# Kernel optimization log

Measured on AMD Instinct MI355X. Metric: run time of the kernel, lower is better.

## Reference

```python
import jax, jax.numpy as jnp
import numpy as np
import math

N_STFT = 1025
N_MELS = 128
SAMPLE_RATE = 16000
F_MIN = 0.0
F_MAX = 8000.0
MAX_ITER = 20
LR = 0.3
MOMENTUM = 0.9
BATCH = 4
TIME = 1024


def _create_fb_matrix(n_freqs, f_min, f_max, n_mels, sample_rate):
    # Triangular mel filterbank, (n_freqs, n_mels), matching torchaudio's create_fb_matrix.
    all_freqs = np.linspace(0.0, sample_rate // 2, n_freqs)
    m_min = 2595.0 * math.log10(1.0 + f_min / 700.0)
    m_max = 2595.0 * math.log10(1.0 + f_max / 700.0)
    m_pts = np.linspace(m_min, m_max, n_mels + 2)
    f_pts = 700.0 * (10.0 ** (m_pts / 2595.0) - 1.0)
    f_diff = f_pts[1:] - f_pts[:-1]
    slopes = f_pts[None, :] - all_freqs[:, None]  # (n_freqs, n_mels+2)
    down_slopes = -slopes[:, :-2] / f_diff[:-1]
    up_slopes = slopes[:, 2:] / f_diff[1:]
    fb = np.maximum(0.0, np.minimum(down_slopes, up_slopes))
    return jnp.asarray(fb, dtype=jnp.float32)


def setup_inputs() -> dict:
    key = jax.random.key(0)
    k1, k2 = jax.random.split(key)
    melspec = jax.random.uniform(k1, (BATCH, N_MELS, TIME), dtype=jnp.float32)
    # torch.rand initialization of the estimated spectrogram, exposed for determinism
    spec_init = jax.random.uniform(k2, (BATCH, TIME, N_STFT), dtype=jnp.float32)
    fb = _create_fb_matrix(N_STFT, F_MIN, F_MAX, N_MELS, SAMPLE_RATE)
    return {"melspec": melspec, "spec_init": spec_init, "fb": fb}


def reference(melspec, spec_init, fb):
    # melspec: (B, n_mels, T) -> (B, T, n_mels); fb: (n_stft, n_mels)
    mel_t = jnp.swapaxes(melspec, -1, -2)
    b, t, _ = mel_t.shape
    inv = 2.0 / (b * t)  # d(mean over B*T of sum_m diff^2)/d(spec) prefactor

    def step(carry, _):
        spec, buf = carry
        diff = mel_t - jnp.einsum('btf,fm->btm', spec, fb)      # (B,T,M)
        grad = -inv * jnp.einsum('btm,fm->btf', diff, fb)       # (B,T,F)
        buf = MOMENTUM * buf + grad                              # SGD momentum buffer
        spec = jnp.maximum(spec - LR * buf, 0.0)                 # update + clamp(min=0)
        return (spec, buf), None

    init = (spec_init, jnp.zeros_like(spec_init))
    (spec, _), _ = jax.lax.scan(step, init, None, length=MAX_ITER)
    return jnp.swapaxes(spec, -1, -2)  # (B, n_stft, T)
```

## Files before the change

kernel.cpp:

```cpp
#include <hip/hip_runtime.h>

#define N_STFT 1025
#define N_MELS 128
#define BATCH 4
#define TIME 1024
#define MAX_ITER 20

__global__ void imel_prep(const float* __restrict__ fb, int* __restrict__ m0f,
                          float* __restrict__ w0a, float* __restrict__ w1a) {
  const int w = threadIdx.x >> 6, l = threadIdx.x & 63;
  const int f = blockIdx.x * 4 + w;
  if (f >= N_STFT) return;
  const float* row = fb + (size_t)f * N_MELS;
  const unsigned long long mlo = __ballot(row[l] != 0.0f);
  const unsigned long long mhi = __ballot(row[l + 64] != 0.0f);
  if (l == 0) {
    int m0 = mlo ? __builtin_ctzll(mlo)
                 : (mhi ? 64 + __builtin_ctzll(mhi) : 0);
    if (m0 > N_MELS - 2) m0 = N_MELS - 2;
    m0f[f] = m0;
    w0a[f] = row[m0];
    w1a[f] = row[m0 + 1];
  }
}

__global__ __launch_bounds__(1024, 8) void imel_main(
    const float* __restrict__ melspec, const float* __restrict__ spec_init,
    const int* __restrict__ m0f, const float* __restrict__ w0a,
    const float* __restrict__ w1a, float* __restrict__ out) {
  __shared__ int   s_PD[4][2 * N_MELS];
  __shared__ float s_out[4][1060];

  const int tid = threadIdx.x;
  const int w   = tid >> 6;
  const int l   = tid & 63;
  const int row = w >> 2;
  const int q   = w & 3;
  const int c   = q * 64 + l;
  const int blk = blockIdx.x;
  const int b   = blk >> 8;
  const int t0  = (blk & 255) << 2;
  const int t   = t0 + row;

  const float SCALE = 16777216.0f;
  const float INV_SCALE = 1.0f / 16777216.0f;

  float rs[4], rb[4], rw0[4], rw1[4];
  int rm[4];

  const float* srow = spec_init + (size_t)(b * TIME + t) * N_STFT;
#pragma unroll
  for (int k = 0; k < 4; ++k) {
    const int f = (c << 2) + k;
    rs[k]  = srow[f];
    rm[k]  = m0f[f];
    rw0[k] = w0a[f] * SCALE;
    rw1[k] = w1a[f] * SCALE;
    rb[k]  = 0.f;
  }
  const bool tail = (c == 255);
  const float rtail = tail ? srow[1024] : 0.f;

  const bool adv1 = (rm[1] != rm[0]);
  const bool adv2 = (rm[2] != rm[1]);
  const bool adv3 = (rm[3] != rm[2]);

  const int dr = (tid >> 7) & 3, dm = tid & 127;
  const bool dact = tid < 512;
  const float GRAD_C = (-2.0f / (BATCH * TIME)) * INV_SCALE;
  const float NC2 = -GRAD_C * INV_SCALE;
  const float melG = dact
      ? GRAD_C * melspec[((size_t)b * N_MELS + dm) * TIME + t0 + dr] : 0.f;

  if (dact) s_PD[dr][dm] = 0;
  __syncthreads();

  for (int it = 0; it < MAX_ITER; ++it) {
    {
      float a0 = rs[0] * rw0[0];
      float a1 = rs[0] * rw1[0];
      if (adv1) atomicAdd(&s_PD[row][rm[0]], __float2int_rn(a0));
      a0 = (adv1 ? a1 : a0) + rs[1] * rw0[1];
      a1 = (adv1 ? 0.f : a1) + rs[1] * rw1[1];
      if (adv2) atomicAdd(&s_PD[row][rm[1]], __float2int_rn(a0));
      a0 = (adv2 ? a1 : a0) + rs[2] * rw0[2];
      a1 = (adv2 ? 0.f : a1) + rs[2] * rw1[2];
      if (adv3) atomicAdd(&s_PD[row][rm[2]], __float2int_rn(a0));
      a0 = (adv3 ? a1 : a0) + rs[3] * rw0[3];
      a1 = (adv3 ? 0.f : a1) + rs[3] * rw1[3];
      atomicAdd(&s_PD[row][rm[3]],     __float2int_rn(a0));
      atomicAdd(&s_PD[row][rm[3] + 1], __float2int_rn(a1));
    }
    __syncthreads();
    if (dact) {
      const float pf = (float)s_PD[dr][dm];
      s_PD[dr][N_MELS + dm] = __float_as_int(fmaf(pf, NC2, melG));
      s_PD[dr][dm] = 0;
    }
    __syncthreads();
    float d0[4], d1[4];
#pragma unroll
    for (int k = 0; k < 4; ++k) {
      d0[k] = __int_as_float(s_PD[row][N_MELS + rm[k]]);
      d1[k] = __int_as_float(s_PD[row][N_MELS + rm[k] + 1]);
    }
#pragma unroll
    for (int k = 0; k < 4; ++k) {
      const float g = fmaf(d1[k], rw1[k], d0[k] * rw0[k]);
      rb[k] = fmaf(0.9f, rb[k], g);
      rs[k] = fmaxf(fmaf(-0.3f, rb[k], rs[k]), 0.f);
    }
  }

#pragma unroll
  for (int k = 0; k < 4; ++k) {
    const int f = (c << 2) + k;
    s_out[row][f + (f >> 5)] = rs[k];
  }
  if (tail) s_out[row][1056] = rtail;
  __syncthreads();

  const int tl = tid & 3;
  const int fg = tid >> 2;
  float* obase = out + (size_t)b * N_STFT * TIME + t0 + tl;
  for (int f = fg; f < N_STFT; f += 256) {
    obase[(size_t)f * TIME] = s_out[tl][f + (f >> 5)];
  }
}

extern "C" void kernel_launch(void* const* d_in, const int* in_sizes, int n_in,
                              void* d_out, int out_size, void* d_ws, size_t ws_size,
                              hipStream_t stream) {
  const float* melspec = (const float*)d_in[0];
  const float* spec_init = (const float*)d_in[1];
  const float* fb = (const float*)d_in[2];
  float* out = (float*)d_out;

  int* m0f = (int*)d_ws;
  float* w0a = (float*)((char*)d_ws + 5120);
  float* w1a = (float*)((char*)d_ws + 10240);

  imel_prep<<<dim3(257), dim3(256), 0, stream>>>(fb, m0f, w0a, w1a);
  imel_main<<<dim3(1024), dim3(1024), 0, stream>>>(melspec, spec_init, m0f, w0a, w1a, out);
}
```

Baseline: 117.1 us.

## Process two time rows per thread with packed 64-bit LDS atomics

Each thread now updates two adjacent time frames, and the two fixed-point mel partial sums are packed into a single 64-bit shared-memory atomic add. Block size halves to 512 threads, and the per-frequency weights and mel indices are reused across both frames. The goal is fewer LDS atomics and fewer threads per unit of work. In exchange, register pressure rises, and carries from a negative low half spill into the high half of the packed sum.

```diff
diff --git a/kernel.cpp b/kernel.cpp
--- a/kernel.cpp
+++ b/kernel.cpp
@@ -5,6 +5,9 @@
 #define BATCH 4
 #define TIME 1024
 #define MAX_ITER 20
+
+typedef unsigned long long u64;
+typedef unsigned int u32;
 
 __global__ void imel_prep(const float* __restrict__ fb, int* __restrict__ m0f,
                           float* __restrict__ w0a, float* __restrict__ w1a) {
@@ -24,106 +27,135 @@
   }
 }
 
-__global__ __launch_bounds__(1024, 8) void imel_main(
+__device__ __forceinline__ u64 pk_rn(float x, float y) {
+  return (u64)(u32)__float2int_rn(x) | ((u64)(u32)__float2int_rn(y) << 32);
+}
+
+__global__ __launch_bounds__(512, 8) void imel_main(
     const float* __restrict__ melspec, const float* __restrict__ spec_init,
     const int* __restrict__ m0f, const float* __restrict__ w0a,
     const float* __restrict__ w1a, float* __restrict__ out) {
-  __shared__ int   s_PD[4][2 * N_MELS];
+  __shared__ u64   s_PD[2][N_MELS][2];
   __shared__ float s_out[4][1060];
 
   const int tid = threadIdx.x;
   const int w   = tid >> 6;
   const int l   = tid & 63;
-  const int row = w >> 2;
+  const int pr  = w >> 2;
   const int q   = w & 3;
   const int c   = q * 64 + l;
   const int blk = blockIdx.x;
   const int b   = blk >> 8;
   const int t0  = (blk & 255) << 2;
-  const int t   = t0 + row;
 
   const float SCALE = 16777216.0f;
   const float INV_SCALE = 1.0f / 16777216.0f;
 
-  float rs[4], rb[4], rw0[4], rw1[4];
+  float rsA[4], rsB[4], rbA[4], rbB[4], rw0[4], rw1[4];
   int rm[4];
 
-  const float* srow = spec_init + (size_t)(b * TIME + t) * N_STFT;
+  const float* srowA = spec_init + (size_t)(b * TIME + t0 + 2 * pr) * N_STFT;
+  const float* srowB = srowA + N_STFT;
 #pragma unroll
   for (int k = 0; k < 4; ++k) {
     const int f = (c << 2) + k;
-    rs[k]  = srow[f];
+    rsA[k] = srowA[f];
+    rsB[k] = srowB[f];
     rm[k]  = m0f[f];
     rw0[k] = w0a[f] * SCALE;
     rw1[k] = w1a[f] * SCALE;
-    rb[k]  = 0.f;
+    rbA[k] = 0.f;
+    rbB[k] = 0.f;
   }
   const bool tail = (c == 255);
-  const float rtail = tail ? srow[1024] : 0.f;
+  const float rtA = tail ? srowA[1024] : 0.f;
+  const float rtB = tail ? srowB[1024] : 0.f;
 
   const bool adv1 = (rm[1] != rm[0]);
   const bool adv2 = (rm[2] != rm[1]);
   const bool adv3 = (rm[3] != rm[2]);
 
-  const int dr = (tid >> 7) & 3, dm = tid & 127;
-  const bool dact = tid < 512;
+  const int dp = (tid >> 7) & 1, dm = tid & 127;
+  const bool dact = tid < 256;
   const float GRAD_C = (-2.0f / (BATCH * TIME)) * INV_SCALE;
   const float NC2 = -GRAD_C * INV_SCALE;
-  const float melG = dact
-      ? GRAD_C * melspec[((size_t)b * N_MELS + dm) * TIME + t0 + dr] : 0.f;
+  float melGlo = 0.f, melGhi = 0.f;
+  if (dact) {
+    const float* mp = melspec + ((size_t)b * N_MELS + dm) * TIME + t0 + 2 * dp;
+    melGlo = GRAD_C * mp[0];
+    melGhi = GRAD_C * mp[1];
+  }
 
-  if (dact) s_PD[dr][dm] = 0;
+  if (dact) s_PD[dp][dm][0] = 0ULL;
   __syncthreads();
 
   for (int it = 0; it < MAX_ITER; ++it) {
     {
-      float a0 = rs[0] * rw0[0];
-      float a1 = rs[0] * rw1[0];
-      if (adv1) atomicAdd(&s_PD[row][rm[0]], __float2int_rn(a0));
-      a0 = (adv1 ? a1 : a0) + rs[1] * rw0[1];
-      a1 = (adv1 ? 0.f : a1) + rs[1] * rw1[1];
-      if (adv2) atomicAdd(&s_PD[row][rm[1]], __float2int_rn(a0));
-      a0 = (adv2 ? a1 : a0) + rs[2] * rw0[2];
-      a1 = (adv2 ? 0.f : a1) + rs[2] * rw1[2];
-      if (adv3) atomicAdd(&s_PD[row][rm[2]], __float2int_rn(a0));
-      a0 = (adv3 ? a1 : a0) + rs[3] * rw0[3];
-      a1 = (adv3 ? 0.f : a1) + rs[3] * rw1[3];
-      atomicAdd(&s_PD[row][rm[3]],     __float2int_rn(a0));
-      atomicAdd(&s_PD[row][rm[3] + 1], __float2int_rn(a1));
+      float a0A = rsA[0] * rw0[0], a1A = rsA[0] * rw1[0];
+      float a0B = rsB[0] * rw0[0], a1B = rsB[0] * rw1[0];
+      if (adv1) atomicAdd(&s_PD[pr][rm[0]][0], pk_rn(a0A, a0B));
+      a0A = (adv1 ? a1A : a0A) + rsA[1] * rw0[1];
+      a1A = (adv1 ? 0.f : a1A) + rsA[1] * rw1[1];
+      a0B = (adv1 ? a1B : a0B) + rsB[1] * rw0[1];
+      a1B = (adv1 ? 0.f : a1B) + rsB[1] * rw1[1];
+      if (adv2) atomicAdd(&s_PD[pr][rm[1]][0], pk_rn(a0A, a0B));
+      a0A = (adv2 ? a1A : a0A) + rsA[2] * rw0[2];
+      a1A = (adv2 ? 0.f : a1A) + rsA[2] * rw1[2];
+      a0B = (adv2 ? a1B : a0B) + rsB[2] * rw0[2];
+      a1B = (adv2 ? 0.f : a1B) + rsB[2] * rw1[2];
+      if (adv3) atomicAdd(&s_PD[pr][rm[2]][0], pk_rn(a0A, a0B));
+      a0A = (adv3 ? a1A : a0A) + rsA[3] * rw0[3];
+      a1A = (adv3 ? 0.f : a1A) + rsA[3] * rw1[3];
+      a0B = (adv3 ? a1B : a0B) + rsB[3] * rw0[3];
+      a1B = (adv3 ? 0.f : a1B) + rsB[3] * rw1[3];
+      atomicAdd(&s_PD[pr][rm[3]][0],     pk_rn(a0A, a0B));
+      atomicAdd(&s_PD[pr][rm[3] + 1][0], pk_rn(a1A, a1B));
     }
     __syncthreads();
     if (dact) {
-      const float pf = (float)s_PD[dr][dm];
-      s_PD[dr][N_MELS + dm] = __float_as_int(fmaf(pf, NC2, melG));
-      s_PD[dr][dm] = 0;
+      const u64 p = s_PD[dp][dm][0];
+      const float plo = (float)(int)(u32)p;
+      const float phi = (float)(int)(u32)(p >> 32);
+      const float dlo = fmaf(plo, NC2, melGlo);
+      const float dhi = fmaf(phi, NC2, melGhi);
+      s_PD[dp][dm][1] = (u64)__float_as_uint(dlo) |
+                        ((u64)__float_as_uint(dhi) << 32);
+      s_PD[dp][dm][0] = 0ULL;
     }
     __syncthreads();
-    float d0[4], d1[4];
 #pragma unroll
     for (int k = 0; k < 4; ++k) {
-      d0[k] = __int_as_float(s_PD[row][N_MELS + rm[k]]);
-      d1[k] = __int_as_float(s_PD[row][N_MELS + rm[k] + 1]);
-    }
-#pragma unroll
-    for (int k = 0; k < 4; ++k) {
-      const float g = fmaf(d1[k], rw1[k], d0[k] * rw0[k]);
-      rb[k] = fmaf(0.9f, rb[k], g);
-      rs[k] = fmaxf(fmaf(-0.3f, rb[k], rs[k]), 0.f);
+      const u64 wd0 = s_PD[pr][rm[k]][1];
+      const u64 wd1 = s_PD[pr][rm[k] + 1][1];
+      const float d0A = __uint_as_float((u32)wd0);
+      const float d0B = __uint_as_float((u32)(wd0 >> 32));
+      const float d1A = __uint_as_float((u32)wd1);
+      const float d1B = __uint_as_float((u32)(wd1 >> 32));
+      const float gA = fmaf(d1A, rw1[k], d0A * rw0[k]);
+      const float gB = fmaf(d1B, rw1[k], d0B * rw0[k]);
+      rbA[k] = fmaf(0.9f, rbA[k], gA);
+      rbB[k] = fmaf(0.9f, rbB[k], gB);
+      rsA[k] = fmaxf(fmaf(-0.3f, rbA[k], rsA[k]), 0.f);
+      rsB[k] = fmaxf(fmaf(-0.3f, rbB[k], rsB[k]), 0.f);
     }
   }
 
 #pragma unroll
   for (int k = 0; k < 4; ++k) {
     const int f = (c << 2) + k;
-    s_out[row][f + (f >> 5)] = rs[k];
+    s_out[2 * pr][f + (f >> 5)]     = rsA[k];
+    s_out[2 * pr + 1][f + (f >> 5)] = rsB[k];
   }
-  if (tail) s_out[row][1056] = rtail;
+  if (tail) {
+    s_out[2 * pr][1056]     = rtA;
+    s_out[2 * pr + 1][1056] = rtB;
+  }
   __syncthreads();
 
   const int tl = tid & 3;
   const int fg = tid >> 2;
   float* obase = out + (size_t)b * N_STFT * TIME + t0 + tl;
-  for (int f = fg; f < N_STFT; f += 256) {
+  for (int f = fg; f < N_STFT; f += 128) {
     obase[(size_t)f * TIME] = s_out[tl][f + (f >> 5)];
   }
 }
@@ -141,5 +173,5 @@
   float* w1a = (float*)((char*)d_ws + 10240);
 
   imel_prep<<<dim3(257), dim3(256), 0, stream>>>(fb, m0f, w0a, w1a);
-  imel_main<<<dim3(1024), dim3(1024), 0, stream>>>(melspec, spec_init, m0f, w0a, w1a, out);
+  imel_main<<<dim3(1024), dim3(512), 0, stream>>>(melspec, spec_init, m0f, w0a, w1a, out);
 }
```

Measured after the change: 119.4 us. No clear change (+1.9%).
